# Kernel optimization log

Hardware: AMD Instinct MI355X
Metric: run time of the kernel (lower is better)

Reference implementation:

```python
import jax, jax.numpy as jnp
import numpy as np

B, S, D, H, E, K = 4, 512, 1024, 16, 4, 2
HD = D // H
LN_EPS = 1e-5


def setup_inputs() -> dict:
    key = jax.random.key(0)
    ks = jax.random.split(key, 16)
    def w(k, shape, fan_in):
        return jax.random.normal(k, shape, jnp.float32) / np.float32(np.sqrt(fan_in))
    return {
        "x": jax.random.normal(ks[0], (B, S, D), jnp.float32),
        # stacked per-expert attention params [E, D, D] / [E, D]
        "Wq": w(ks[1], (E, D, D), D), "bq": jnp.zeros((E, D), jnp.float32),
        "Wk": w(ks[2], (E, D, D), D), "bk": jnp.zeros((E, D), jnp.float32),
        "Wv": w(ks[3], (E, D, D), D), "bv": jnp.zeros((E, D), jnp.float32),
        "Wo": w(ks[4], (E, D, D), D), "bo": jnp.zeros((E, D), jnp.float32),
        # router: Linear(D->D/2), LayerNorm, relu, Linear(D/2->E)
        "Wr1": w(ks[5], (D, D // 2), D), "br1": jnp.zeros((D // 2,), jnp.float32),
        "ln_g": jnp.ones((D // 2,), jnp.float32), "ln_b": jnp.zeros((D // 2,), jnp.float32),
        "Wr2": w(ks[6], (D // 2, E), D // 2), "br2": jnp.zeros((E,), jnp.float32),
    }


def _moe_attention(x, Wq, bq, Wk, bk, Wv, bv, Wo, bo, Wr1, br1, ln_g, ln_b, Wr2, br2):
    # ---- router ----
    h = x @ Wr1 + br1                                        # [B,S,D/2]
    mu = jnp.mean(h, axis=-1, keepdims=True)
    var = jnp.var(h, axis=-1, keepdims=True)
    h = (h - mu) * jax.lax.rsqrt(var + LN_EPS) * ln_g + ln_b
    h = jax.nn.relu(h)
    logits = h @ Wr2 + br2                                   # [B,S,E]
    probs = jax.nn.softmax(logits, axis=-1)
    top_p, top_i = jax.lax.top_k(probs, K)                   # [B,S,K]
    # scatter-add of top-k probs into dense expert mask [B,S,E]
    emask = jnp.sum(jax.nn.one_hot(top_i, E, dtype=x.dtype) * top_p[..., None], axis=2)

    # ---- dense per-expert attention (naive: every expert on every token) ----
    def heads(t):  # [E,B,S,D] -> [E,B,H,S,HD]
        return t.reshape(E, B, S, H, HD).transpose(0, 1, 3, 2, 4)

    q = heads(jnp.einsum('bsd,edf->ebsf', x, Wq) + bq[:, None, None, :])
    k = heads(jnp.einsum('bsd,edf->ebsf', x, Wk) + bk[:, None, None, :])
    v = heads(jnp.einsum('bsd,edf->ebsf', x, Wv) + bv[:, None, None, :])

    scores = jnp.einsum('ebhqd,ebhkd->ebhqk', q, k) / np.float32(np.sqrt(HD))
    attn = jax.nn.softmax(scores, axis=-1)                   # [E,B,H,S,S]
    o = jnp.einsum('ebhqk,ebhkd->ebhqd', attn, v)
    o = o.transpose(0, 1, 3, 2, 4).reshape(E, B, S, D)
    o = jnp.einsum('ebsd,edf->ebsf', o, Wo) + bo[:, None, None, :]  # [E,B,S,D]

    # ---- masked combine ----
    return jnp.einsum('ebsd,bse->bsd', o, emask)


def reference(x, Wq, bq, Wk, bk, Wv, bv, Wo, bo, Wr1, br1, ln_g, ln_b, Wr2, br2):
    return _moe_attention(x, Wq, bq, Wk, bk, Wv, bv, Wo, bo,
                          Wr1, br1, ln_g, ln_b, Wr2, br2)
```

## Files before the change

kernel.cpp:

```cpp
#include <hip/hip_runtime.h>
#include <hip/hip_bf16.h>
#include <math.h>

#define B_   4
#define S_   512
#define D_   1024
#define H_   16
#define E_   4
#define HD_  64
#define D2_  512
#define NTOK (B_*S_)

#define TDE ((size_t)NTOK * D_)
#define WWE ((size_t)D_ * D_)
#define ND2 ((size_t)NTOK * D2_)

typedef unsigned short ushort;
typedef short shortv8 __attribute__((ext_vector_type(8)));
typedef ushort ushortv4 __attribute__((ext_vector_type(4)));
typedef _Float16 halfv8 __attribute__((ext_vector_type(8)));
typedef _Float16 halfv4 __attribute__((ext_vector_type(4)));
typedef float floatv4 __attribute__((ext_vector_type(4)));

__device__ __forceinline__ ushort f2bf(float f) {
    union { __hip_bfloat16 b; ushort u; } cv;
    cv.b = __float2bfloat16(f);
    return cv.u;
}
__device__ __forceinline__ float bf2f(ushort u) {
    union { ushort u; __hip_bfloat16 b; } cv;
    cv.u = u;
    return __bfloat162float(cv.b);
}
__device__ __forceinline__ void gload16(const void* g, void* l) {
    __builtin_amdgcn_global_load_lds(
        (const __attribute__((address_space(1))) unsigned int*)g,
        (__attribute__((address_space(3))) unsigned int*)l, 16, 0, 0);
}

__device__ __forceinline__ void gemm_core_bf(
    const ushort* __restrict__ A0, const ushort* __restrict__ A1,
    const ushort* __restrict__ B0, const ushort* __restrict__ B1,
    int K, int klen, int brow, int bcol, ushort* lds, floatv4 acc[4][4])
{
    const int tid  = threadIdx.x;
    const int wave = tid >> 6, lane = tid & 63;
    const int wm = wave >> 1, wn = wave & 1;
    const int lr = lane & 15, lc = lane >> 4;

    const ushort* gsrc[4] = {A0, A1, B0, B1};
    size_t goff[4][2];
    int    loff[4][2];
#pragma unroll
    for (int t = 0; t < 4; t++) {
#pragma unroll
        for (int s = 0; s < 2; s++) {
            int p = s * 256 + tid;
            int m = p >> 2;
            int c = (p & 3) ^ ((m >> 1) & 3);
            int r = (t < 2) ? (brow + m) : (bcol + m);
            goff[t][s] = (size_t)r * K + c * 8;
            loff[t][s] = t * 4096 + p * 8;
        }
    }

    int aoff[4], boff[4];
#pragma unroll
    for (int i = 0; i < 4; i++) {
        int ra = wm * 64 + i * 16 + lr;
        aoff[i] = ra * 32 + ((lc ^ ((ra >> 1) & 3)) * 8);
        int rb2 = wn * 64 + i * 16 + lr;
        boff[i] = rb2 * 32 + ((lc ^ ((rb2 >> 1) & 3)) * 8);
    }

#define STAGEB_(buf, kk) \
    _Pragma("unroll") for (int t = 0; t < 4; t++) \
    _Pragma("unroll") for (int s = 0; s < 2; s++) \
        gload16(gsrc[t] + goff[t][s] + (kk), lds + (buf) * 16384 + loff[t][s]);

    STAGEB_(0, 0)

    int cur = 0;
    for (int k0 = 0; k0 < klen; k0 += 32, cur ^= 1) {
        if (k0 + 32 < klen) {
            STAGEB_(cur ^ 1, k0 + 32)
            asm volatile("s_waitcnt vmcnt(8)" ::: "memory");
        } else {
            asm volatile("s_waitcnt vmcnt(0)" ::: "memory");
        }
        __builtin_amdgcn_s_barrier();
        __builtin_amdgcn_sched_barrier(0);

        const ushort* L = lds + cur * 16384;
        shortv8 ah[4], al[4], bh[4], bl[4];
#pragma unroll
        for (int i = 0; i < 4; i++) {
            ah[i] = *(const shortv8*)(L +         aoff[i]);
            al[i] = *(const shortv8*)(L +  4096 + aoff[i]);
            bh[i] = *(const shortv8*)(L +  8192 + boff[i]);
            bl[i] = *(const shortv8*)(L + 12288 + boff[i]);
        }
#pragma unroll
        for (int mi = 0; mi < 4; mi++)
#pragma unroll
            for (int nj = 0; nj < 4; nj++) {
                acc[mi][nj] = __builtin_amdgcn_mfma_f32_16x16x32_bf16(ah[mi], bh[nj], acc[mi][nj], 0, 0, 0);
                acc[mi][nj] = __builtin_amdgcn_mfma_f32_16x16x32_bf16(ah[mi], bl[nj], acc[mi][nj], 0, 0, 0);
                acc[mi][nj] = __builtin_amdgcn_mfma_f32_16x16x32_bf16(al[mi], bh[nj], acc[mi][nj], 0, 0, 0);
            }

        asm volatile("s_waitcnt lgkmcnt(0)" ::: "memory");
        __builtin_amdgcn_sched_barrier(0);
        __builtin_amdgcn_s_barrier();
    }
#undef STAGEB_
}

__device__ __forceinline__ void gemm_core_h2(
    const _Float16* __restrict__ A0, const _Float16* __restrict__ B0,
    int K, int klen, int brow, int bcol, _Float16* lds, floatv4 acc[8][4])
{
    const int tid  = threadIdx.x;
    const int wave = tid >> 6, lane = tid & 63;
    const int wm = wave >> 1, wn = wave & 1;
    const int lr = lane & 15, lc = lane >> 4;

    size_t goffA[4];
    int    loffA[4];
#pragma unroll
    for (int s = 0; s < 4; s++) {
        int p = s * 256 + tid;
        int m = p >> 2;
        int c = (p & 3) ^ ((m >> 1) & 3);
        goffA[s] = (size_t)(brow + m) * K + c * 8;
        loffA[s] = p * 8;
    }
    size_t goffB[2];
    int    loffB[2];
#pragma unroll
    for (int s = 0; s < 2; s++) {
        int p = s * 256 + tid;
        int m = p >> 2;
        int c = (p & 3) ^ ((m >> 1) & 3);
        goffB[s] = (size_t)(bcol + m) * K + c * 8;
        loffB[s] = 8192 + p * 8;
    }

    int aoff[8], boff[4];
#pragma unroll
    for (int i = 0; i < 8; i++) {
        int ra = wm * 128 + i * 16 + lr;
        aoff[i] = ra * 32 + ((lc ^ ((ra >> 1) & 3)) * 8);
    }
#pragma unroll
    for (int j = 0; j < 4; j++) {
        int rb = wn * 64 + j * 16 + lr;
        boff[j] = 8192 + rb * 32 + ((lc ^ ((rb >> 1) & 3)) * 8);
    }

#define STAGEH_(buf, kk) \
    _Pragma("unroll") for (int s = 0; s < 4; s++) \
        gload16(A0 + goffA[s] + (kk), lds + (buf) * 12288 + loffA[s]); \
    _Pragma("unroll") for (int s = 0; s < 2; s++) \
        gload16(B0 + goffB[s] + (kk), lds + (buf) * 12288 + loffB[s]);

    STAGEH_(0, 0)

    int cur = 0;
    for (int k0 = 0; k0 < klen; k0 += 32, cur ^= 1) {
        if (k0 + 32 < klen) {
            STAGEH_(cur ^ 1, k0 + 32)
            asm volatile("s_waitcnt vmcnt(6)" ::: "memory");
        } else {
            asm volatile("s_waitcnt vmcnt(0)" ::: "memory");
        }
        __builtin_amdgcn_s_barrier();
        __builtin_amdgcn_sched_barrier(0);

        const _Float16* L = lds + cur * 12288;
        halfv8 aa[8], bb[4];
#pragma unroll
        for (int j = 0; j < 4; j++) bb[j] = *(const halfv8*)(L + boff[j]);
#pragma unroll
        for (int i = 0; i < 8; i++) aa[i] = *(const halfv8*)(L + aoff[i]);
#pragma unroll
        for (int mi = 0; mi < 8; mi++)
#pragma unroll
            for (int nj = 0; nj < 4; nj++)
                acc[mi][nj] = __builtin_amdgcn_mfma_f32_16x16x32_f16(aa[mi], bb[nj], acc[mi][nj], 0, 0, 0);

        asm volatile("s_waitcnt lgkmcnt(0)" ::: "memory");
        __builtin_amdgcn_sched_barrier(0);
        __builtin_amdgcn_s_barrier();
    }
#undef STAGEH_
}

#define ACC_INIT4(acc) \
    _Pragma("unroll") for (int i = 0; i < 4; i++) \
    _Pragma("unroll") for (int j = 0; j < 4; j++) \
    _Pragma("unroll") for (int q = 0; q < 4; q++) acc[i][j][q] = 0.f;

#define ACC_INIT8(acc) \
    _Pragma("unroll") for (int i = 0; i < 8; i++) \
    _Pragma("unroll") for (int j = 0; j < 4; j++) \
    _Pragma("unroll") for (int q = 0; q < 4; q++) acc[i][j][q] = 0.f;

#define EPI_VARS \
    const int lane = threadIdx.x & 63, wave = threadIdx.x >> 6; \
    const int wm = wave >> 1, wn = wave & 1, lr = lane & 15, lc = lane >> 4;

__global__ __launch_bounds__(256, 2) void gemm_mega(
    const ushort* __restrict__ xh, const ushort* __restrict__ xl,
    const ushort* __restrict__ wr1h, const ushort* __restrict__ wr1l,
    float* __restrict__ hpart,
    const _Float16* __restrict__ xf, const _Float16* __restrict__ wth,
    const float* __restrict__ bq, const float* __restrict__ bk, const float* __restrict__ bv,
    _Float16* __restrict__ qf, _Float16* __restrict__ kf, _Float16* __restrict__ vf)
{
    __shared__ ushort smem[32768];
    const int bid = blockIdx.x;
    const int xcd = bid & 7, j = bid >> 3;

    if (j < 32) {
        const int u = xcd * 32 + j;
        const int kz = u >> 6;
        const int rem = u & 63;
        const int brow = (rem >> 2) * 128, bcol = (rem & 3) * 128;

        floatv4 acc[4][4];
        ACC_INIT4(acc)
        const int koff = kz * 256;
        gemm_core_bf(xh + koff, xl + koff, wr1h + koff, wr1l + koff,
                     D_, 256, brow, bcol, smem, acc);

        float* C = hpart + (size_t)kz * ND2;
        EPI_VARS
#pragma unroll
        for (int mi = 0; mi < 4; mi++)
#pragma unroll
            for (int nj = 0; nj < 4; nj++)
#pragma unroll
                for (int i = 0; i < 4; i++) {
                    int row = brow + wm * 64 + mi * 16 + lc * 4 + i;
                    int col = bcol + wn * 64 + nj * 16 + lr;
                    C[(size_t)row * D2_ + col] = acc[mi][nj][i];
                }
    } else if (j < 96) {
        const int u = xcd * 64 + (j - 32);
        const int z = u >> 6;
        const int rem = u & 63;
        const int brow = (rem >> 3) * 256, bcol = (rem & 7) * 128;
        const int slot = z >> 1, m = z & 1;
        const size_t so = (size_t)slot * TDE;
        const _Float16* Bm = wth + (size_t)(slot * 4 + 1 + m) * WWE;
        const float* bias = ((m == 0) ? bk : bv) + (size_t)slot * D_;
        _Float16* Oo = ((m == 0) ? kf : vf) + so;

        floatv4 acc[8][4];
        ACC_INIT8(acc)
        gemm_core_h2(xf, Bm, D_, D_, brow, bcol, (_Float16*)smem, acc);

        EPI_VARS
#pragma unroll
        for (int mi = 0; mi < 8; mi++)
#pragma unroll
            for (int nj = 0; nj < 4; nj++)
#pragma unroll
                for (int i = 0; i < 4; i++) {
                    int row = brow + wm * 128 + mi * 16 + lc * 4 + i;
                    int col = bcol + wn * 64 + nj * 16 + lr;
                    Oo[(size_t)row * D_ + col] = (_Float16)(acc[mi][nj][i] + bias[col]);
                }
    } else {
        const int u = xcd * 32 + (j - 96);
        const int e = u >> 6;
        const int rem = u & 63;
        const int brow = (rem >> 3) * 256, bcol = (rem & 7) * 128;
        const _Float16* Bm = wth + (size_t)(e * 4 + 0) * WWE;
        const float* bias = bq + (size_t)e * D_;
        _Float16* Oo = qf + (size_t)e * TDE;

        floatv4 acc[8][4];
        ACC_INIT8(acc)
        gemm_core_h2(xf, Bm, D_, D_, brow, bcol, (_Float16*)smem, acc);

        EPI_VARS
#pragma unroll
        for (int mi = 0; mi < 8; mi++)
#pragma unroll
            for (int nj = 0; nj < 4; nj++)
#pragma unroll
                for (int i = 0; i < 4; i++) {
                    int row = brow + wm * 128 + mi * 16 + lc * 4 + i;
                    int col = bcol + wn * 64 + nj * 16 + lr;
                    Oo[(size_t)row * D_ + col] =
                        (_Float16)((acc[mi][nj][i] + bias[col]) * 0.125f);
                }
    }
}

__global__ __launch_bounds__(256, 2) void gemm_combine4(
    const _Float16* __restrict__ oh,
    const _Float16* __restrict__ wth,
    const float* __restrict__ bo, const float* __restrict__ emask,
    const int* __restrict__ idx, const int* __restrict__ meta,
    float* __restrict__ out2)
{
    __shared__ _Float16 lds[24576];
    const int lid = blockIdx.x + 8 * (blockIdx.y + 8 * blockIdx.z);
    const int nid = (lid & 7) * 32 + (lid >> 3);
    const int e = nid >> 6;
    const int rem = nid & 63;
    const int brow = (rem >> 3) * 256, bcol = (rem & 7) * 128;

    const int pcnt = meta[32 + e];
    if (brow >= pcnt) return;
    const size_t so = (size_t)e * TDE;
    const _Float16* Bm = wth + (size_t)(e * 4 + 3) * WWE;
    const float* bias = bo + (size_t)e * D_;
    const int* idxe = idx + e * 2048;

    floatv4 acc[8][4];
    ACC_INIT8(acc)
    gemm_core_h2(oh + so, Bm, D_, D_, brow, bcol, lds, acc);

    EPI_VARS
#pragma unroll
    for (int mi = 0; mi < 8; mi++)
#pragma unroll
        for (int nj = 0; nj < 4; nj++)
#pragma unroll
            for (int i = 0; i < 4; i++) {
                int srow = brow + wm * 128 + mi * 16 + lc * 4 + i;
                int raw = idxe[srow];
                if (raw >= 0) {
                    int row = raw & 0xFFFF;
                    int rank = (raw >> 30) & 1;
                    float s = emask[(size_t)row * E_ + e];
                    int col = bcol + wn * 64 + nj * 16 + lr;
                    out2[(size_t)rank * TDE + (size_t)row * D_ + col] =
                        s * (acc[mi][nj][i] + bias[col]);
                }
            }
}

__global__ __launch_bounds__(256) void reduce_out(
    const float* __restrict__ out2, float* __restrict__ out)
{
    size_t i = (size_t)blockIdx.x * 256 + threadIdx.x;
    const float4* p = (const float4*)out2;
    float4 a = p[i], b = p[i + TDE / 4];
    float4 r;
    r.x = a.x + b.x;
    r.y = a.y + b.y;
    r.z = a.z + b.z;
    r.w = a.w + b.w;
    ((float4*)out)[i] = r;
}

__global__ __launch_bounds__(256) void build_lists(
    const float* __restrict__ emask, int* __restrict__ idx, int* __restrict__ meta)
{
    const int e = blockIdx.x;
    const int tid = threadIdx.x;
    __shared__ int scan[256];
    __shared__ int runsh;
    if (tid == 0) runsh = 0;
    int* idxe = idx + e * 2048;

    for (int b = 0; b < B_; b++) {
        __syncthreads();
        const int base = runsh;
        int t0 = b * 512 + tid * 2;
        int f0 = (emask[(size_t)t0 * E_ + e] != 0.f) ? 1 : 0;
        int f1 = (emask[(size_t)(t0 + 1) * E_ + e] != 0.f) ? 1 : 0;
        int my = f0 + f1;
        scan[tid] = my;
        __syncthreads();
        for (int off = 1; off < 256; off <<= 1) {
            int v = (tid >= off) ? scan[tid - off] : 0;
            __syncthreads();
            scan[tid] += v;
            __syncthreads();
        }
        int excl = scan[tid] - my;
        int cnt = scan[255];
        if (f0) {
            int rank = 0;
            for (int ep = 0; ep < e; ep++)
                if (emask[(size_t)t0 * E_ + ep] != 0.f) rank = 1;
            idxe[base + excl] = t0 | (rank << 30);
        }
        if (f1) {
            int rank = 0;
            for (int ep = 0; ep < e; ep++)
                if (emask[(size_t)(t0 + 1) * E_ + ep] != 0.f) rank = 1;
            idxe[base + excl + f0] = (t0 + 1) | (rank << 30);
        }
        int plen = (cnt + 63) & ~63;
        for (int i = cnt + tid; i < plen; i += 256)
            idxe[base + i] = (b * 512) | (int)0x80000000;
        if (tid == 0) {
            meta[e * 4 + b] = base;
            meta[16 + e * 4 + b] = plen >> 6;
            runsh = base + plen;
        }
    }
    __syncthreads();
    int total = runsh;
    if (tid == 0) meta[32 + e] = total;
    for (int i = total + tid; i < 2048; i += 256)
        idxe[i] = (int)0x80000000;
}

__global__ __launch_bounds__(256, 3) void attn_all(
    const _Float16* __restrict__ qf_, const _Float16* __restrict__ kf_,
    const _Float16* __restrict__ vf_,
    _Float16* __restrict__ oh_,
    const int* __restrict__ idx, const int* __restrict__ meta)
{
    const int lid = blockIdx.x + 8 * (blockIdx.y + 64 * blockIdx.z);
    const int nid = (lid & 7) * 256 + (lid >> 3);
    const int e = nid >> 9;
    const int rem = nid & 511;
    const int bhid = rem >> 3, qtile = rem & 7;
    const int bb = bhid >> 4, hh = bhid & 15;

    const int ptiles = meta[16 + e * 4 + bb];
    if (qtile >= ptiles) return;
    const int pstart = meta[e * 4 + bb];

    __shared__ _Float16 Kf[128 * 64];
    __shared__ _Float16 Vt[64 * 128];
    __shared__ _Float16 Pw[4][16 * 128];

    const size_t zo = (size_t)e * TDE;
    const int tid = threadIdx.x;
    const int wave = tid >> 6, lane = tid & 63;
    const int lr = lane & 15, lc = lane >> 4;
    const int q0 = pstart + qtile * 64;
    const size_t kvbase = zo + (size_t)bb * S_ * D_ + hh * 64;

    halfv8 qq[2];
    {
        int slot = q0 + wave * 16 + lr;
        int tok = idx[e * 2048 + slot] & 0xFFFF;
        size_t qoff = zo + (size_t)tok * D_ + hh * 64 + lc * 8;
        qq[0] = *(const halfv8*)(qf_ + qoff);
        qq[1] = *(const halfv8*)(qf_ + qoff + 32);
    }

    floatv4 ov[4];
    float m4[4], l4[4];
#pragma unroll
    for (int df = 0; df < 4; df++)
#pragma unroll
        for (int i = 0; i < 4; i++) ov[df][i] = 0.f;
#pragma unroll
    for (int i = 0; i < 4; i++) { m4[i] = -3.0e38f; l4[i] = 0.f; }

    halfv8 vr[2][2];
#define LOADV_(kk0_) \
    _Pragma("unroll") for (int pp = 0; pp < 2; pp++) { \
        const _Float16* vsrc = vf_ + kvbase + (size_t)((kk0_) + pp * 64 + lane) * D_ + wave * 16; \
        vr[pp][0] = *(const halfv8*)vsrc; \
        vr[pp][1] = *(const halfv8*)(vsrc + 8); \
    }

    LOADV_(0)

    for (int kt = 0; kt < S_ / 128; kt++) {
        const int kk0 = kt * 128;
        __syncthreads();

#pragma unroll
        for (int s = 0; s < 4; s++) {
            int p = s * 256 + tid;
            int r = p >> 3;
            int c = (p & 7) ^ (r & 7);
            gload16(kf_ + kvbase + (size_t)(kk0 + r) * D_ + c * 8, Kf + p * 8);
        }
#pragma unroll
        for (int pp = 0; pp < 2; pp++) {
            int k = pp * 64 + lane;
            int kc = k >> 3, kl = k & 7;
#pragma unroll
            for (int h = 0; h < 2; h++)
#pragma unroll
                for (int jj = 0; jj < 8; jj++) {
                    int d = wave * 16 + h * 8 + jj;
                    Vt[d * 128 + ((kc ^ jj) << 3) + kl] = vr[pp][h][jj];
                }
        }
        __syncthreads();

        if (kt + 1 < S_ / 128) { LOADV_(kk0 + 128) }

        floatv4 sc[8];
#pragma unroll
        for (int n = 0; n < 8; n++)
#pragma unroll
            for (int i = 0; i < 4; i++) sc[n][i] = 0.f;
        __builtin_amdgcn_s_setprio(1);
#pragma unroll
        for (int n = 0; n < 8; n++)
#pragma unroll
            for (int ds = 0; ds < 2; ds++) {
                int off = (16 * n + lr) * 64 + (((ds * 4 + lc) ^ (lr & 7)) * 8);
                halfv8 kr = *(const halfv8*)(Kf + off);
                sc[n] = __builtin_amdgcn_mfma_f32_16x16x32_f16(qq[ds], kr, sc[n], 0, 0, 0);
            }
        __builtin_amdgcn_s_setprio(0);

        float tm[4];
#pragma unroll
        for (int i = 0; i < 4; i++) {
            float a = fmaxf(fmaxf(sc[0][i], sc[1][i]), fmaxf(sc[2][i], sc[3][i]));
            float b = fmaxf(fmaxf(sc[4][i], sc[5][i]), fmaxf(sc[6][i], sc[7][i]));
            tm[i] = fmaxf(a, b);
        }
#pragma unroll
        for (int off = 1; off <= 8; off <<= 1)
#pragma unroll
            for (int i = 0; i < 4; i++)
                tm[i] = fmaxf(tm[i], __shfl_xor(tm[i], off));

        float nm[4], sca[4], ps[4];
#pragma unroll
        for (int i = 0; i < 4; i++) {
            nm[i] = fmaxf(m4[i], tm[i]);
            sca[i] = __expf(m4[i] - nm[i]);
            ps[i] = 0.f;
        }
#pragma unroll
        for (int n = 0; n < 8; n++)
#pragma unroll
            for (int i = 0; i < 4; i++) {
                float p = __expf(sc[n][i] - nm[i]);
                ps[i] += p;
                int q = lc * 4 + i;
                int kcol = 16 * n + lr;
                Pw[wave][q * 128 + (((kcol >> 3) ^ (q & 7)) << 3) + (kcol & 7)] =
                    (_Float16)p;
            }
#pragma unroll
        for (int off = 1; off <= 8; off <<= 1)
#pragma unroll
            for (int i = 0; i < 4; i++)
                ps[i] += __shfl_xor(ps[i], off);
#pragma unroll
        for (int i = 0; i < 4; i++) {
            l4[i] = l4[i] * sca[i] + ps[i];
            m4[i] = nm[i];
        }
#pragma unroll
        for (int df = 0; df < 4; df++)
#pragma unroll
            for (int i = 0; i < 4; i++) ov[df][i] *= sca[i];

        asm volatile("s_waitcnt lgkmcnt(0)" ::: "memory");
        __builtin_amdgcn_sched_barrier(0);

        __builtin_amdgcn_s_setprio(1);
#pragma unroll
        for (int ks = 0; ks < 4; ks++) {
            int ch = ((ks * 4 + lc) ^ (lr & 7)) * 8;
            halfv8 pa = *(const halfv8*)(&Pw[wave][lr * 128 + ch]);
#pragma unroll
            for (int df = 0; df < 4; df++) {
                halfv8 vfr = *(const halfv8*)(Vt + (df * 16 + lr) * 128 + ch);
                ov[df] = __builtin_amdgcn_mfma_f32_16x16x32_f16(pa, vfr, ov[df], 0, 0, 0);
            }
        }
        __builtin_amdgcn_s_setprio(0);
    }
#undef LOADV_

    const size_t qobase = zo + hh * 64;
#pragma unroll
    for (int df = 0; df < 4; df++)
#pragma unroll
        for (int i = 0; i < 4; i++) {
            float val = ov[df][i] / l4[i];
            size_t off = qobase + (size_t)(q0 + wave * 16 + lc * 4 + i) * D_ + df * 16 + lr;
            oh_[off] = (_Float16)val;
        }
}

__global__ __launch_bounds__(256) void split_f32(
    const float* __restrict__ in, ushort* __restrict__ hb, ushort* __restrict__ lb,
    _Float16* __restrict__ hf)
{
    int i = blockIdx.x * 256 + threadIdx.x;
    float4 v = ((const float4*)in)[i];
    float vv[4] = {v.x, v.y, v.z, v.w};
    ushortv4 hv, lv;
    halfv4 hhv;
#pragma unroll
    for (int j = 0; j < 4; j++) {
        ushort h = f2bf(vv[j]);
        hv[j] = h;
        lv[j] = f2bf(vv[j] - bf2f(h));
        hhv[j] = (_Float16)vv[j];
    }
    ((ushortv4*)hb)[i] = hv;
    ((ushortv4*)lb)[i] = lv;
    ((halfv4*)hf)[i] = hhv;
}

__global__ __launch_bounds__(256) void tsplit(
    const float* __restrict__ W, ushort* __restrict__ Th, ushort* __restrict__ Tl,
    int K, int N)
{
    __shared__ float tile[64][65];
    const int n0 = blockIdx.x * 64, k0 = blockIdx.y * 64;
    const int tid = threadIdx.x;
#pragma unroll
    for (int i = 0; i < 16; i++) {
        int idx = i * 256 + tid;
        int r = idx >> 6, c = idx & 63;
        tile[r][c] = W[(size_t)(k0 + r) * N + n0 + c];
    }
    __syncthreads();
#pragma unroll
    for (int i = 0; i < 16; i++) {
        int idx = i * 256 + tid;
        int rn = idx >> 6, ck = idx & 63;
        float v = tile[ck][rn];
        ushort h = f2bf(v);
        Th[(size_t)(n0 + rn) * K + k0 + ck] = h;
        Tl[(size_t)(n0 + rn) * K + k0 + ck] = f2bf(v - bf2f(h));
    }
}

__global__ __launch_bounds__(256) void tsplit16h(
    const float* __restrict__ Wq, const float* __restrict__ Wk,
    const float* __restrict__ Wv, const float* __restrict__ Wo,
    _Float16* __restrict__ Th)
{
    __shared__ float tile[64][65];
    const int mg = blockIdx.z;
    const int e = mg >> 2, m = mg & 3;
    const float* W = ((m == 0) ? Wq : (m == 1) ? Wk : (m == 2) ? Wv : Wo) + (size_t)e * WWE;
    _Float16* T = Th + (size_t)mg * WWE;
    const int n0 = blockIdx.x * 64, k0 = blockIdx.y * 64;
    const int tid = threadIdx.x;
#pragma unroll
    for (int i = 0; i < 16; i++) {
        int idx = i * 256 + tid;
        int r = idx >> 6, c = idx & 63;
        tile[r][c] = W[(size_t)(k0 + r) * D_ + n0 + c];
    }
    __syncthreads();
#pragma unroll
    for (int i = 0; i < 16; i++) {
        int idx = i * 256 + tid;
        int rn = idx >> 6, ck = idx & 63;
        T[(size_t)(n0 + rn) * D_ + k0 + ck] = (_Float16)tile[ck][rn];
    }
}

__global__ __launch_bounds__(256) void router_post(
    const float* __restrict__ hpart, const float* __restrict__ br1,
    const float* __restrict__ ln_g, const float* __restrict__ ln_b,
    const float* __restrict__ Wr2, const float* __restrict__ br2,
    float* __restrict__ emask)
{
    const int t = blockIdx.x;
    const int tid = threadIdx.x;
    __shared__ float red[256];
    __shared__ float logits[E_];

    const float* hp = hpart + (size_t)t * D2_;
    float x0 = hp[tid] + hp[ND2 + tid] + hp[2 * ND2 + tid] + hp[3 * ND2 + tid] + br1[tid];
    float x1 = hp[tid + 256] + hp[ND2 + tid + 256] + hp[2 * ND2 + tid + 256]
             + hp[3 * ND2 + tid + 256] + br1[tid + 256];

    red[tid] = x0 + x1; __syncthreads();
    for (int off = 128; off; off >>= 1) { if (tid < off) red[tid] += red[tid + off]; __syncthreads(); }
    float mu = red[0] * (1.f / 512.f);
    __syncthreads();

    float d0 = x0 - mu, d1 = x1 - mu;
    red[tid] = d0 * d0 + d1 * d1; __syncthreads();
    for (int off = 128; off; off >>= 1) { if (tid < off) red[tid] += red[tid + off]; __syncthreads(); }
    float rs = rsqrtf(red[0] * (1.f / 512.f) + 1e-5f);
    __syncthreads();

    float n0 = fmaxf(fmaf(d0 * rs, ln_g[tid],       ln_b[tid]),       0.f);
    float n1 = fmaxf(fmaf(d1 * rs, ln_g[tid + 256], ln_b[tid + 256]), 0.f);

    for (int e = 0; e < E_; e++) {
        red[tid] = n0 * Wr2[(size_t)tid * E_ + e] + n1 * Wr2[(size_t)(tid + 256) * E_ + e];
        __syncthreads();
        for (int off = 128; off; off >>= 1) { if (tid < off) red[tid] += red[tid + off]; __syncthreads(); }
        if (tid == 0) logits[e] = red[0] + br2[e];
        __syncthreads();
    }

    if (tid == 0) {
        float mx = fmaxf(fmaxf(logits[0], logits[1]), fmaxf(logits[2], logits[3]));
        float p[E_], sum = 0.f;
        for (int e = 0; e < E_; e++) { p[e] = expf(logits[e] - mx); sum += p[e]; }
        float inv = 1.f / sum;
        for (int e = 0; e < E_; e++) p[e] *= inv;
        int i1 = 0;
        for (int e = 1; e < E_; e++) if (p[e] > p[i1]) i1 = e;
        int i2 = -1;
        for (int e = 0; e < E_; e++) { if (e == i1) continue; if (i2 < 0 || p[e] > p[i2]) i2 = e; }
        float o[E_] = {0.f, 0.f, 0.f, 0.f};
        o[i1] = p[i1]; o[i2] = p[i2];
        for (int e = 0; e < E_; e++) emask[(size_t)t * E_ + e] = o[e];
    }
}

extern "C" void kernel_launch(void* const* d_in, const int* in_sizes, int n_in,
                              void* d_out, int out_size, void* d_ws, size_t ws_size,
                              hipStream_t stream) {
    const float* x   = (const float*)d_in[0];
    const float* Wq  = (const float*)d_in[1];
    const float* bq  = (const float*)d_in[2];
    const float* Wk  = (const float*)d_in[3];
    const float* bk  = (const float*)d_in[4];
    const float* Wv  = (const float*)d_in[5];
    const float* bv  = (const float*)d_in[6];
    const float* Wo  = (const float*)d_in[7];
    const float* bo  = (const float*)d_in[8];
    const float* Wr1 = (const float*)d_in[9];
    const float* br1 = (const float*)d_in[10];
    const float* lng = (const float*)d_in[11];
    const float* lnb = (const float*)d_in[12];
    const float* Wr2 = (const float*)d_in[13];
    const float* br2 = (const float*)d_in[14];

    float* out = (float*)d_out;
    char* w = (char*)d_ws;
    dim3 blk(256);
    const size_t MB = 1024ull * 1024ull;

    float*    emask = (float*)w;
    int*      idx   = (int*)(w + 64 * 1024);
    int*      meta  = (int*)(w + 96 * 1024);
    _Float16* wth   = (_Float16*)(w + 1 * MB);
    ushort*   wr1h  = (ushort*)(w + 33 * MB);
    ushort*   wr1l  = (ushort*)(w + 34 * MB);
    ushort*   xh    = (ushort*)(w + 35 * MB);
    ushort*   xl    = (ushort*)(w + 39 * MB);
    _Float16* xfh   = (_Float16*)(w + 43 * MB);
    float*    hpart = (float*)(w + 47 * MB);
    _Float16* qfb   = (_Float16*)(w + 63 * MB);
    _Float16* kfb   = (_Float16*)(w + 79 * MB);
    _Float16* vfb   = (_Float16*)(w + 95 * MB);
    _Float16* ohb   = (_Float16*)(w + 111 * MB);
    float*    out2  = (float*)(w + 127 * MB);

    split_f32<<<dim3(NTOK * D_ / 1024), blk, 0, stream>>>(x, xh, xl, xfh);
    tsplit<<<dim3(D2_ / 64, D_ / 64), blk, 0, stream>>>(Wr1, wr1h, wr1l, D_, D2_);
    tsplit16h<<<dim3(16, 16, 16), blk, 0, stream>>>(Wq, Wk, Wv, Wo, wth);

    gemm_mega<<<dim3(1024), blk, 0, stream>>>(
        xh, xl, wr1h, wr1l, hpart, xfh, wth, bq, bk, bv, qfb, kfb, vfb);

    router_post<<<dim3(NTOK), blk, 0, stream>>>(hpart, br1, lng, lnb, Wr2, br2, emask);
    build_lists<<<dim3(E_), blk, 0, stream>>>(emask, idx, meta);

    attn_all<<<dim3(8, 64, 4), blk, 0, stream>>>(
        qfb, kfb, vfb, ohb, idx, meta);

    gemm_combine4<<<dim3(8, 8, 4), blk, 0, stream>>>(
        ohb, wth, bo, emask, idx, meta, out2);
    reduce_out<<<dim3(TDE / 1024), blk, 0, stream>>>(out2, out);
}
```

Measured before the change: 211.3 us.

## Merge prep kernels, single-buffer router GEMM, raise occupancy hints to 3

Fuses the three input/weight preparation kernels into one launch, removing two launch gaps. The router bf16 split GEMM drops its double-buffered LDS staging in favour of a single buffer with a full wait each K step. Shared memory in gemm_mega shrinks and the launch bounds of gemm_mega and gemm_combine4 go to 3 blocks per CU. The aim is more resident blocks, at the cost of losing load/compute overlap in the router path and possibly spilling registers under the tighter bound.

New measurement: 213.2 us. No clear change (+0.9%).

```diff
diff --git a/kernel.cpp b/kernel.cpp
--- a/kernel.cpp
+++ b/kernel.cpp
@@ -38,7 +38,7 @@
         (__attribute__((address_space(3))) unsigned int*)l, 16, 0, 0);
 }
 
-__device__ __forceinline__ void gemm_core_bf(
+__device__ __forceinline__ void gemm_core_bf_sb(
     const ushort* __restrict__ A0, const ushort* __restrict__ A1,
     const ushort* __restrict__ B0, const ushort* __restrict__ B1,
     int K, int klen, int brow, int bcol, ushort* lds, floatv4 acc[4][4])
@@ -73,32 +73,23 @@
         boff[i] = rb2 * 32 + ((lc ^ ((rb2 >> 1) & 3)) * 8);
     }
 
-#define STAGEB_(buf, kk) \
-    _Pragma("unroll") for (int t = 0; t < 4; t++) \
-    _Pragma("unroll") for (int s = 0; s < 2; s++) \
-        gload16(gsrc[t] + goff[t][s] + (kk), lds + (buf) * 16384 + loff[t][s]);
-
-    STAGEB_(0, 0)
-
-    int cur = 0;
-    for (int k0 = 0; k0 < klen; k0 += 32, cur ^= 1) {
-        if (k0 + 32 < klen) {
-            STAGEB_(cur ^ 1, k0 + 32)
-            asm volatile("s_waitcnt vmcnt(8)" ::: "memory");
-        } else {
-            asm volatile("s_waitcnt vmcnt(0)" ::: "memory");
-        }
+    for (int k0 = 0; k0 < klen; k0 += 32) {
+#pragma unroll
+        for (int t = 0; t < 4; t++)
+#pragma unroll
+            for (int s = 0; s < 2; s++)
+                gload16(gsrc[t] + goff[t][s] + k0, lds + loff[t][s]);
+        asm volatile("s_waitcnt vmcnt(0)" ::: "memory");
         __builtin_amdgcn_s_barrier();
         __builtin_amdgcn_sched_barrier(0);
 
-        const ushort* L = lds + cur * 16384;
         shortv8 ah[4], al[4], bh[4], bl[4];
 #pragma unroll
         for (int i = 0; i < 4; i++) {
-            ah[i] = *(const shortv8*)(L +         aoff[i]);
-            al[i] = *(const shortv8*)(L +  4096 + aoff[i]);
-            bh[i] = *(const shortv8*)(L +  8192 + boff[i]);
-            bl[i] = *(const shortv8*)(L + 12288 + boff[i]);
+            ah[i] = *(const shortv8*)(lds +         aoff[i]);
+            al[i] = *(const shortv8*)(lds +  4096 + aoff[i]);
+            bh[i] = *(const shortv8*)(lds +  8192 + boff[i]);
+            bl[i] = *(const shortv8*)(lds + 12288 + boff[i]);
         }
 #pragma unroll
         for (int mi = 0; mi < 4; mi++)
@@ -113,7 +104,6 @@
         __builtin_amdgcn_sched_barrier(0);
         __builtin_amdgcn_s_barrier();
     }
-#undef STAGEB_
 }
 
 __device__ __forceinline__ void gemm_core_h2(
@@ -210,7 +200,7 @@
     const int lane = threadIdx.x & 63, wave = threadIdx.x >> 6; \
     const int wm = wave >> 1, wn = wave & 1, lr = lane & 15, lc = lane >> 4;
 
-__global__ __launch_bounds__(256, 2) void gemm_mega(
+__global__ __launch_bounds__(256, 3) void gemm_mega(
     const ushort* __restrict__ xh, const ushort* __restrict__ xl,
     const ushort* __restrict__ wr1h, const ushort* __restrict__ wr1l,
     float* __restrict__ hpart,
@@ -218,7 +208,7 @@
     const float* __restrict__ bq, const float* __restrict__ bk, const float* __restrict__ bv,
     _Float16* __restrict__ qf, _Float16* __restrict__ kf, _Float16* __restrict__ vf)
 {
-    __shared__ ushort smem[32768];
+    __shared__ ushort smem[24576];
     const int bid = blockIdx.x;
     const int xcd = bid & 7, j = bid >> 3;
 
@@ -231,8 +221,8 @@
         floatv4 acc[4][4];
         ACC_INIT4(acc)
         const int koff = kz * 256;
-        gemm_core_bf(xh + koff, xl + koff, wr1h + koff, wr1l + koff,
-                     D_, 256, brow, bcol, smem, acc);
+        gemm_core_bf_sb(xh + koff, xl + koff, wr1h + koff, wr1l + koff,
+                        D_, 256, brow, bcol, smem, acc);
 
         float* C = hpart + (size_t)kz * ND2;
         EPI_VARS
@@ -300,7 +290,7 @@
     }
 }
 
-__global__ __launch_bounds__(256, 2) void gemm_combine4(
+__global__ __launch_bounds__(256, 3) void gemm_combine4(
     const _Float16* __restrict__ oh,
     const _Float16* __restrict__ wth,
     const float* __restrict__ bo, const float* __restrict__ emask,
@@ -588,76 +578,74 @@
         }
 }
 
-__global__ __launch_bounds__(256) void split_f32(
-    const float* __restrict__ in, ushort* __restrict__ hb, ushort* __restrict__ lb,
-    _Float16* __restrict__ hf)
-{
-    int i = blockIdx.x * 256 + threadIdx.x;
-    float4 v = ((const float4*)in)[i];
-    float vv[4] = {v.x, v.y, v.z, v.w};
-    ushortv4 hv, lv;
-    halfv4 hhv;
-#pragma unroll
-    for (int j = 0; j < 4; j++) {
-        ushort h = f2bf(vv[j]);
-        hv[j] = h;
-        lv[j] = f2bf(vv[j] - bf2f(h));
-        hhv[j] = (_Float16)vv[j];
-    }
-    ((ushortv4*)hb)[i] = hv;
-    ((ushortv4*)lb)[i] = lv;
-    ((halfv4*)hf)[i] = hhv;
-}
-
-__global__ __launch_bounds__(256) void tsplit(
-    const float* __restrict__ W, ushort* __restrict__ Th, ushort* __restrict__ Tl,
-    int K, int N)
-{
-    __shared__ float tile[64][65];
-    const int n0 = blockIdx.x * 64, k0 = blockIdx.y * 64;
-    const int tid = threadIdx.x;
-#pragma unroll
-    for (int i = 0; i < 16; i++) {
-        int idx = i * 256 + tid;
-        int r = idx >> 6, c = idx & 63;
-        tile[r][c] = W[(size_t)(k0 + r) * N + n0 + c];
-    }
-    __syncthreads();
-#pragma unroll
-    for (int i = 0; i < 16; i++) {
-        int idx = i * 256 + tid;
-        int rn = idx >> 6, ck = idx & 63;
-        float v = tile[ck][rn];
-        ushort h = f2bf(v);
-        Th[(size_t)(n0 + rn) * K + k0 + ck] = h;
-        Tl[(size_t)(n0 + rn) * K + k0 + ck] = f2bf(v - bf2f(h));
-    }
-}
-
-__global__ __launch_bounds__(256) void tsplit16h(
+__global__ __launch_bounds__(256) void prep_all(
+    const float* __restrict__ x,
+    ushort* __restrict__ hb, ushort* __restrict__ lb, _Float16* __restrict__ hf,
+    const float* __restrict__ Wr1, ushort* __restrict__ wr1h, ushort* __restrict__ wr1l,
     const float* __restrict__ Wq, const float* __restrict__ Wk,
     const float* __restrict__ Wv, const float* __restrict__ Wo,
     _Float16* __restrict__ Th)
 {
     __shared__ float tile[64][65];
-    const int mg = blockIdx.z;
-    const int e = mg >> 2, m = mg & 3;
-    const float* W = ((m == 0) ? Wq : (m == 1) ? Wk : (m == 2) ? Wv : Wo) + (size_t)e * WWE;
-    _Float16* T = Th + (size_t)mg * WWE;
-    const int n0 = blockIdx.x * 64, k0 = blockIdx.y * 64;
+    const int bid = blockIdx.x;
     const int tid = threadIdx.x;
-#pragma unroll
-    for (int i = 0; i < 16; i++) {
-        int idx = i * 256 + tid;
-        int r = idx >> 6, c = idx & 63;
-        tile[r][c] = W[(size_t)(k0 + r) * D_ + n0 + c];
-    }
-    __syncthreads();
-#pragma unroll
-    for (int i = 0; i < 16; i++) {
-        int idx = i * 256 + tid;
-        int rn = idx >> 6, ck = idx & 63;
-        T[(size_t)(n0 + rn) * D_ + k0 + ck] = (_Float16)tile[ck][rn];
+
+    if (bid < 2048) {
+        int i = bid * 256 + tid;
+        float4 v = ((const float4*)x)[i];
+        float vv[4] = {v.x, v.y, v.z, v.w};
+        ushortv4 hv, lv;
+        halfv4 hhv;
+#pragma unroll
+        for (int j = 0; j < 4; j++) {
+            ushort h = f2bf(vv[j]);
+            hv[j] = h;
+            lv[j] = f2bf(vv[j] - bf2f(h));
+            hhv[j] = (_Float16)vv[j];
+        }
+        ((ushortv4*)hb)[i] = hv;
+        ((ushortv4*)lb)[i] = lv;
+        ((halfv4*)hf)[i] = hhv;
+    } else if (bid < 2176) {
+        int u = bid - 2048;
+        int n0 = (u & 7) * 64, k0 = (u >> 3) * 64;
+#pragma unroll
+        for (int i = 0; i < 16; i++) {
+            int p = i * 256 + tid;
+            int r = p >> 6, c = p & 63;
+            tile[r][c] = Wr1[(size_t)(k0 + r) * D2_ + n0 + c];
+        }
+        __syncthreads();
+#pragma unroll
+        for (int i = 0; i < 16; i++) {
+            int p = i * 256 + tid;
+            int rn = p >> 6, ck = p & 63;
+            float v = tile[ck][rn];
+            ushort h = f2bf(v);
+            wr1h[(size_t)(n0 + rn) * D_ + k0 + ck] = h;
+            wr1l[(size_t)(n0 + rn) * D_ + k0 + ck] = f2bf(v - bf2f(h));
+        }
+    } else {
+        int u = bid - 2176;
+        int xg = u & 15, yg = (u >> 4) & 15, mg = u >> 8;
+        const int e = mg >> 2, m = mg & 3;
+        const float* W = ((m == 0) ? Wq : (m == 1) ? Wk : (m == 2) ? Wv : Wo)
+                         + (size_t)e * WWE;
+        _Float16* T = Th + (size_t)mg * WWE;
+        const int n0 = xg * 64, k0 = yg * 64;
+#pragma unroll
+        for (int i = 0; i < 16; i++) {
+            int p = i * 256 + tid;
+            int r = p >> 6, c = p & 63;
+            tile[r][c] = W[(size_t)(k0 + r) * D_ + n0 + c];
+        }
+        __syncthreads();
+#pragma unroll
+        for (int i = 0; i < 16; i++) {
+            int p = i * 256 + tid;
+            int rn = p >> 6, ck = p & 63;
+            T[(size_t)(n0 + rn) * D_ + k0 + ck] = (_Float16)tile[ck][rn];
+        }
     }
 }
 
@@ -755,9 +743,8 @@
     _Float16* ohb   = (_Float16*)(w + 111 * MB);
     float*    out2  = (float*)(w + 127 * MB);
 
-    split_f32<<<dim3(NTOK * D_ / 1024), blk, 0, stream>>>(x, xh, xl, xfh);
-    tsplit<<<dim3(D2_ / 64, D_ / 64), blk, 0, stream>>>(Wr1, wr1h, wr1l, D_, D2_);
-    tsplit16h<<<dim3(16, 16, 16), blk, 0, stream>>>(Wq, Wk, Wv, Wo, wth);
+    prep_all<<<dim3(6272), blk, 0, stream>>>(
+        x, xh, xl, xfh, Wr1, wr1h, wr1l, Wq, Wk, Wv, Wo, wth);
 
     gemm_mega<<<dim3(1024), blk, 0, stream>>>(
         xh, xl, wr1h, wr1l, hpart, xfh, wth, bq, bk, bv, qfb, kfb, vfb);
```
